# Performance work log

Hardware: AMD Instinct MI355X
Metric: run time of the kernel (lower is better)

The kernel has to match this reference:

```python
import jax, jax.numpy as jnp
from jax import lax
import numpy as np

LATENT = 512
LABEL = 128
BATCH = 1024


def _maxpool2(x):
    # 2x2 max pool, stride 2, NCHW
    return lax.reduce_window(x, -jnp.inf, lax.max, (1, 1, 2, 2), (1, 1, 2, 2), 'VALID')


def _encoder(x, c1w, c1b, c2w, c2b, fw, fb):
    dn = ('NCHW', 'OIHW', 'NCHW')
    y = lax.conv_general_dilated(x, c1w, (1, 1), 'SAME', dimension_numbers=dn)
    y = _maxpool2(jax.nn.relu(y + c1b[None, :, None, None]))  # [B,32,14,14]
    y = lax.conv_general_dilated(y, c2w, (1, 1), 'SAME', dimension_numbers=dn)
    y = _maxpool2(jax.nn.relu(y + c2b[None, :, None, None]))  # [B,64,7,7]
    y = y.reshape(y.shape[0], -1)                              # [B,3136]
    return y @ fw.T + fb                                       # [B,latent]


def _hopfield_w(rep):
    # rho = mean over ALL elements (matches torch.mean(x))
    rho = jnp.mean(rep)
    t = rep - rho                      # [label, latent]
    w = t.T @ t                        # sum of rank-1 outer products
    w = w * (1.0 - jnp.eye(w.shape[0], dtype=w.dtype))  # zero diagonal
    return w / LABEL


def _clustering(lat, w):
    # batched fixed-length Hopfield relaxation with min-energy tracking
    s0 = jnp.tanh(lat)                 # [B,L]
    B = s0.shape[0]

    def step(carry, _):
        s, min_e, min_s = carry
        prev = lax.stop_gradient(s)    # torch detaches prev_s each iter
        s_new = jnp.abs(prev) * jnp.sign(prev @ w.T)      # [B,L]
        e = -jnp.einsum('bi,ij,bj->b', s_new, w, s_new)    # [B]
        better = e < min_e
        min_e = jnp.where(better, e, min_e)
        min_s = jnp.where(better[:, None], s_new, min_s)
        return (s_new, min_e, min_s), None

    init = (s0, jnp.full((B,), jnp.inf, dtype=s0.dtype), jnp.zeros_like(s0))
    (_, _, min_s), _ = lax.scan(step, init, None, length=LATENT)
    return min_s


def setup_inputs() -> dict:
    key = jax.random.key(0)
    ks = jax.random.split(key, 11)
    d = {}
    d['image'] = jax.random.normal(ks[0], (BATCH, 1, 28, 28), dtype=jnp.float32)
    d['label_images'] = jax.random.uniform(ks[1], (LABEL, 1, 28, 28), dtype=jnp.float32)
    d['conv1_w'] = jax.random.normal(ks[2], (32, 1, 5, 5), dtype=jnp.float32) * 0.1
    d['conv1_b'] = jnp.zeros((32,), dtype=jnp.float32)
    d['conv2_w'] = jax.random.normal(ks[3], (64, 32, 5, 5), dtype=jnp.float32) * 0.05
    d['conv2_b'] = jnp.zeros((64,), dtype=jnp.float32)
    d['fc1_w'] = jax.random.normal(ks[4], (LATENT, 64 * 7 * 7), dtype=jnp.float32) * 0.02
    d['fc1_b'] = jnp.zeros((LATENT,), dtype=jnp.float32)
    d['fcn_w'] = jax.random.normal(ks[5], (LABEL, LATENT), dtype=jnp.float32) * 0.05
    d['fcn_b'] = jnp.zeros((LABEL,), dtype=jnp.float32)
    return d


def reference(image, label_images, conv1_w, conv1_b, conv2_w, conv2_b,
              fc1_w, fc1_b, fcn_w, fcn_b):
    rep = jnp.tanh(_encoder(label_images, conv1_w, conv1_b, conv2_w, conv2_b, fc1_w, fc1_b))  # [label,L]
    lat = _encoder(image, conv1_w, conv1_b, conv2_w, conv2_b, fc1_w, fc1_b)                    # [B,L]
    # FCN on detached latents (torch: .clone().detach())
    label = jax.nn.softmax(lax.stop_gradient(lat) @ fcn_w.T + fcn_b, axis=1)                   # [B,label]
    w = _hopfield_w(rep)                                                                        # [L,L]
    min_s = _clustering(lat, w)                                                                 # [B,L]
    out = jax.nn.softmax(jnp.abs(min_s @ rep.T), axis=1)                                        # [B,label]
    return (out, label)
```

## Files before the change

### kernel.cpp

```cpp
#include <hip/hip_runtime.h>
#include <hip/hip_bf16.h>
#include <math.h>

#define BATCH 1024
#define LABEL 128
#define LATENT 512
#define NTOT 1152

typedef short short8 __attribute__((ext_vector_type(8)));
typedef float f32x16 __attribute__((ext_vector_type(16)));

__device__ __forceinline__ unsigned short f2bf(float f) {
    __hip_bfloat16 h = __float2bfloat16(f);
    return *(unsigned short*)&h;
}
__device__ __forceinline__ float bf2f(unsigned short u) {
    __hip_bfloat16 h; *(unsigned short*)&h = u;
    return __bfloat162float(h);
}


__global__ __launch_bounds__(256) void conv1_pool(const float* __restrict__ image,
                                                  const float* __restrict__ limg,
                                                  const float* __restrict__ wt,
                                                  const float* __restrict__ bias,
                                                  unsigned short* __restrict__ o1b) {
    const int n = blockIdx.x;
    const float* in = (n < BATCH) ? (image + (size_t)n * 784)
                                  : (limg + (size_t)(n - BATCH) * 784);
    __shared__ float pin[32][32];
    __shared__ float wts[32 * 25];
    const int tid = threadIdx.x;
    unsigned short* ob = o1b + (size_t)n * 12800;
    for (int i = tid; i < 256; i += 256) {
        int pl_ = i >> 7, r = i & 127;
        ob[pl_ * 6400 + 6272 + r] = 0;
    }
    for (int idx = tid; idx < 32 * 32; idx += 256) ((float*)pin)[idx] = 0.f;
    __syncthreads();
    for (int idx = tid; idx < 784; idx += 256) {
        int y = idx / 28, x = idx % 28;
        pin[y + 2][x + 2] = in[idx];
    }
    for (int idx = tid; idx < 800; idx += 256) wts[idx] = wt[idx];
    __syncthreads();
    const int oc = tid & 31;
    float wk[25];
    #pragma unroll
    for (int k = 0; k < 25; ++k) wk[k] = wts[oc * 25 + k];
    float b = bias[oc];
    const int slot_lo = (oc & 7);
    const int gq = oc >> 3;
    for (int o = tid; o < 6272; o += 256) {
        int p = o >> 5, py = p / 14, px = p % 14;
        float win[6][6];
        #pragma unroll
        for (int r = 0; r < 6; ++r)
        #pragma unroll
        for (int c = 0; c < 6; ++c)
            win[r][c] = pin[2 * py + r][2 * px + c];
        float a00 = b, a01 = b, a10 = b, a11 = b;
        #pragma unroll
        for (int ky = 0; ky < 5; ++ky)
        #pragma unroll
        for (int kx = 0; kx < 5; ++kx) {
            float w = wk[ky * 5 + kx];
            a00 = fmaf(win[ky][kx], w, a00);
            a01 = fmaf(win[ky][kx + 1], w, a01);
            a10 = fmaf(win[ky + 1][kx], w, a10);
            a11 = fmaf(win[ky + 1][kx + 1], w, a11);
        }
        float v = fmaxf(fmaxf(fmaxf(a00, a01), fmaxf(a10, a11)), 0.f);
        unsigned short b1 = f2bf(v); float r1 = v - bf2f(b1);
        unsigned short b2 = f2bf(r1);
        int off = p * 32 + (((gq ^ (p >> 1)) & 3) << 3) + slot_lo;
        ob[off] = b1; ob[6400 + off] = b2;
    }
}

#define BSTR ((size_t)512 * 3136)
#define ASTR ((size_t)NTOT * 3136)
__global__ __launch_bounds__(256) void prep(const float* __restrict__ c2w,
                                            const float* __restrict__ f1w,
                                            unsigned short* __restrict__ Bf,
                                            unsigned short* __restrict__ Bw2) {
    int idx = blockIdx.x * 256 + threadIdx.x;
    if (idx < 102400) {
        int j = idx & 7, lane = (idx >> 3) & 63, ocT = (idx >> 9) & 1, s = idx >> 10;
        int q = lane >> 5, nn = lane & 31;
        int k = 16 * s + 8 * q + j;
        int tap = k >> 5, ic = k & 31;
        int oc = 32 * ocT + nn;
        float v = c2w[oc * 800 + ic * 25 + tap];
        unsigned short b1 = f2bf(v);
        unsigned short b2 = f2bf(v - bf2f(b1));
        size_t base = ((size_t)(s * 2 + ocT) * 2) * 512 + lane * 8 + j;
        Bf[base] = b1; Bf[base + 512] = b2;
        return;
    }
    int i2 = idx - 102400;
    if (i2 >= 512 * 3136) return;
    float v = f1w[i2];
    unsigned short b1 = f2bf(v);
    unsigned short b2 = f2bf(v - bf2f(b1));
    Bw2[i2] = b1; Bw2[BSTR + i2] = b2;
}

__global__ __launch_bounds__(256) void conv2_mfma(const unsigned short* __restrict__ o1b,
                                                  const unsigned short* __restrict__ Bf,
                                                  const float* __restrict__ bias,
                                                  unsigned short* __restrict__ out2) {
    const int n = blockIdx.x;
    __shared__ __align__(16) unsigned short pl[12800];
    const int tid = threadIdx.x;
    const int lane = tid & 63, wv = tid >> 6;
    const int ocT = wv & 1, mh = wv >> 1;

    {
        const float4* src = (const float4*)(o1b + (size_t)n * 12800);
        float4* dst = (float4*)pl;
        for (int i = tid; i < 1600; i += 256) dst[i] = src[i];
    }
    __syncthreads();

    const int m_ = lane & 31, q = lane >> 5;
    int ym[4], xm[4], mm[4], tvv[4];
    #pragma unroll
    for (int tt = 0; tt < 4; ++tt) {
        int t = 4 * mh + tt;
        tvv[tt] = (t < 7);
        int m = 32 * t + m_;
        mm[tt] = m;
        ym[tt] = m / 14;
        xm[tt] = m - 14 * ym[tt];
    }
    f32x16 acc[4];
    {
        float bs = bias[32 * ocT + m_];
        #pragma unroll
        for (int tt = 0; tt < 4; ++tt)
        #pragma unroll
        for (int r = 0; r < 16; ++r) acc[tt][r] = bs;
    }

    for (int s = 0; s < 50; ++s) {
        const unsigned short* bp = Bf + ((size_t)(s * 2 + ocT) * 2) * 512 + lane * 8;
        short8 b1 = *(const short8*)(bp);
        short8 b2 = *(const short8*)(bp + 512);
        int kb = 16 * s + 8 * q;
        int tap = kb >> 5, ic0 = kb & 31, g = ic0 >> 3;
        int ky = (tap * 13) >> 6;
        int kx = tap - ky * 5;
        int iyk = ky - 2, ixk = kx - 2;
        int pq2 = iyk * 14 + ixk;
        short8 a1[4], a2[4];
        #pragma unroll
        for (int tt = 0; tt < 4; ++tt) {
            int iy = ym[tt] + iyk, ix = xm[tt] + ixk;
            int valid = tvv[tt] & ((unsigned)iy < 14u) & ((unsigned)ix < 14u);
            int cpt = valid ? (mm[tt] + pq2) : 196;
            int addr = cpt * 32 + (((g ^ (cpt >> 1)) & 3) << 3);
            a1[tt] = *(const short8*)(pl + addr);
            a2[tt] = *(const short8*)(pl + 6400 + addr);
        }
        #pragma unroll
        for (int tt = 0; tt < 4; ++tt)
            acc[tt] = __builtin_amdgcn_mfma_f32_32x32x16_bf16(a1[tt], b1, acc[tt], 0, 0, 0);
        #pragma unroll
        for (int tt = 0; tt < 4; ++tt)
            acc[tt] = __builtin_amdgcn_mfma_f32_32x32x16_bf16(a1[tt], b2, acc[tt], 0, 0, 0);
        #pragma unroll
        for (int tt = 0; tt < 4; ++tt)
            acc[tt] = __builtin_amdgcn_mfma_f32_32x32x16_bf16(a2[tt], b1, acc[tt], 0, 0, 0);
    }
    __syncthreads();

    float* hx = (float*)pl;
    {
        const int oc = 32 * ocT + m_;
        #pragma unroll
        for (int tt = 0; tt < 4; ++tt)
        #pragma unroll
        for (int e = 0; e < 8; ++e) {
            const int reg = 2 * e;
            const int r = (reg & 3) + 8 * (reg >> 2) + 4 * q;
            const int m = 32 * (4 * mh + tt) + r;
            if (m < 196) {
                float xm2 = fmaxf(acc[tt][reg], acc[tt][reg + 1]);
                int y = (m * 2341) >> 15;
                int px = (m - 14 * y) >> 1;
                hx[(y * 7 + px) * 65 + oc] = xm2;
            }
        }
    }
    __syncthreads();

    for (int idx = tid; idx < 3136; idx += 256) {
        int oc2 = (idx * 2675) >> 17;
        int p = idx - 49 * oc2;
        int py = (p * 9363) >> 16;
        int px = p - 7 * py;
        float v = fmaxf(hx[(2 * py * 7 + px) * 65 + oc2],
                        hx[((2 * py + 1) * 7 + px) * 65 + oc2]);
        v = fmaxf(v, 0.f);
        unsigned short b1 = f2bf(v);
        unsigned short b2 = f2bf(v - bf2f(b1));
        size_t o = (size_t)n * 3136 + idx;
        out2[o] = b1; out2[ASTR + o] = b2;
    }
}

__global__ __launch_bounds__(256) void fc1_mfma(const unsigned short* __restrict__ A2,
                                                const unsigned short* __restrict__ B2,
                                                float* __restrict__ part) {
    __shared__ unsigned short As[2][2048];
    __shared__ unsigned short Bs[2][2048];
    const int tid = threadIdx.x;
    const int n0 = blockIdx.x * 64, m0 = blockIdx.y * 64;
    const int koff = blockIdx.z * 448;
    const int lr = tid >> 2, g = tid & 3;
    const int slot = (((g ^ (lr >> 1)) & 3) << 3);
    const int lane = tid & 63, wv = tid >> 6;
    const int nq = wv & 1, mq = wv >> 1;
    const int q = lane >> 5, l31 = lane & 31;
    const int rA = 32 * nq + l31, rB = 32 * mq + l31;
    f32x16 acc;
    #pragma unroll
    for (int r = 0; r < 16; ++r) acc[r] = 0.f;

    for (int bk = 0; bk < 448; bk += 32) {
        const size_t ka = (size_t)(koff + bk + (g << 3));
        short8 av[2], bv[2];
        #pragma unroll
        for (int p = 0; p < 2; ++p) {
            av[p] = *(const short8*)(A2 + p * ASTR + (size_t)(n0 + lr) * 3136 + ka);
            bv[p] = *(const short8*)(B2 + p * BSTR + (size_t)(m0 + lr) * 3136 + ka);
        }
        __syncthreads();
        #pragma unroll
        for (int p = 0; p < 2; ++p) {
            *(short8*)&As[p][(lr << 5) + slot] = av[p];
            *(short8*)&Bs[p][(lr << 5) + slot] = bv[p];
        }
        __syncthreads();
        #pragma unroll
        for (int s2 = 0; s2 < 32; s2 += 16) {
            const int gg = (s2 + (q << 3)) >> 3;
            const int sa = (((gg ^ (rA >> 1)) & 3) << 3);
            const int sb = (((gg ^ (rB >> 1)) & 3) << 3);
            short8 a1 = *(const short8*)&As[0][(rA << 5) + sa];
            short8 a2 = *(const short8*)&As[1][(rA << 5) + sa];
            short8 b1 = *(const short8*)&Bs[0][(rB << 5) + sb];
            short8 b2 = *(const short8*)&Bs[1][(rB << 5) + sb];
            acc = __builtin_amdgcn_mfma_f32_32x32x16_bf16(a1, b1, acc, 0, 0, 0);
            acc = __builtin_amdgcn_mfma_f32_32x32x16_bf16(a1, b2, acc, 0, 0, 0);
            acc = __builtin_amdgcn_mfma_f32_32x32x16_bf16(a2, b1, acc, 0, 0, 0);
        }
    }
    float* pb = part + (size_t)blockIdx.z * NTOT * 512;
    #pragma unroll
    for (int reg = 0; reg < 16; ++reg) {
        int nn = n0 + 32 * nq + (reg & 3) + 8 * (reg >> 2) + 4 * q;
        int mmo = m0 + 32 * mq + l31;
        pb[(size_t)nn * 512 + mmo] = acc[reg];
    }
}

__global__ __launch_bounds__(256) void fc1_reduce(const float* __restrict__ part,
                                                  const float* __restrict__ bias,
                                                  float* __restrict__ lat,
                                                  float* __restrict__ rep) {
    int idx = blockIdx.x * 256 + threadIdx.x;
    int m = idx & 511;
    float v = bias[m];
    #pragma unroll
    for (int kz = 0; kz < 7; ++kz) v += part[(size_t)kz * NTOT * 512 + idx];
    if (idx < BATCH * 512) lat[idx] = v;
    else rep[idx - BATCH * 512] = tanhf(v);
}

__global__ __launch_bounds__(128) void fcn_softmax(const float* __restrict__ lat,
                                                   const float* __restrict__ fw,
                                                   const float* __restrict__ fb,
                                                   float* __restrict__ out) {
    const int b = blockIdx.x;
    const int j = threadIdx.x;
    __shared__ float lrow[512];
    __shared__ float red[128];
    for (int i = j; i < 512; i += 128) lrow[i] = lat[b * 512 + i];
    __syncthreads();
    const float4* w4 = (const float4*)(fw + j * 512);
    float acc = fb[j];
    #pragma unroll 4
    for (int qq = 0; qq < 128; ++qq) {
        float4 a = ((const float4*)lrow)[qq];
        float4 w = w4[qq];
        acc += a.x * w.x + a.y * w.y + a.z * w.z + a.w * w.w;
    }
    red[j] = acc;
    __syncthreads();
    for (int off = 64; off >= 1; off >>= 1) {
        if (j < off) red[j] = fmaxf(red[j], red[j + off]);
        __syncthreads();
    }
    float mx = red[0];
    __syncthreads();
    float ex = expf(acc - mx);
    red[j] = ex;
    __syncthreads();
    for (int off = 64; off >= 1; off >>= 1) {
        if (j < off) red[j] += red[j + off];
        __syncthreads();
    }
    out[b * 128 + j] = ex / red[0];
}

__global__ __launch_bounds__(256) void rho_kernel(const float* __restrict__ rep,
                                                  float* __restrict__ rho) {
    __shared__ float red[256];
    const int tid = threadIdx.x;
    float s = 0.f;
    for (int i = tid; i < LABEL * LATENT; i += 256) s += rep[i];
    red[tid] = s;
    __syncthreads();
    for (int off = 128; off >= 1; off >>= 1) {
        if (tid < off) red[tid] += red[tid + off];
        __syncthreads();
    }
    if (tid == 0) rho[0] = red[0] / (float)(LABEL * LATENT);
}

__global__ __launch_bounds__(256) void t_kernel(const float* __restrict__ rep,
                                                const float* __restrict__ rho,
                                                float* __restrict__ tT) {
    int idx = blockIdx.x * 256 + threadIdx.x;
    int i = idx / 128, k = idx % 128;
    tT[idx] = rep[k * 512 + i] - rho[0];
}

__global__ __launch_bounds__(256) void w_kernel(const float* __restrict__ tT,
                                                float* __restrict__ w) {
    int idx = blockIdx.x * 256 + threadIdx.x;
    int i = idx >> 9, j = idx & 511;
    const float4* a = (const float4*)(tT + i * 128);
    const float4* b = (const float4*)(tT + j * 128);
    float acc = 0.f;
    #pragma unroll 8
    for (int q = 0; q < 32; ++q) {
        float4 av = a[q], bv = b[q];
        acc += av.x * bv.x + av.y * bv.y + av.z * bv.z + av.w * bv.w;
    }
    w[idx] = (i == j) ? 0.f : acc * (1.f / 128.f);
}

__global__ __launch_bounds__(256) void hinit(const float* __restrict__ lat,
                                             const float* __restrict__ w,
                                             float* __restrict__ hmat) {
    __shared__ float As[16][68];
    __shared__ float Bs[16][68];
    const int tid = threadIdx.x;
    const int n0 = blockIdx.x * 64, m0 = blockIdx.y * 64;
    const int lr = tid >> 2;
    const int lk = (tid & 3) * 4;
    const int ty = tid >> 4, tx = tid & 15;
    float c[4][4] = {};
    for (int k0 = 0; k0 < 512; k0 += 16) {
        float4 a4 = *(const float4*)(lat + (size_t)(n0 + lr) * 512 + k0 + lk);
        float4 b4 = *(const float4*)(w + (size_t)(m0 + lr) * 512 + k0 + lk);
        a4.x = tanhf(a4.x); a4.y = tanhf(a4.y); a4.z = tanhf(a4.z); a4.w = tanhf(a4.w);
        __syncthreads();
        As[lk + 0][lr] = a4.x; As[lk + 1][lr] = a4.y; As[lk + 2][lr] = a4.z; As[lk + 3][lr] = a4.w;
        Bs[lk + 0][lr] = b4.x; Bs[lk + 1][lr] = b4.y; Bs[lk + 2][lr] = b4.z; Bs[lk + 3][lr] = b4.w;
        __syncthreads();
        #pragma unroll
        for (int kk = 0; kk < 16; ++kk) {
            float av[4], bv[4];
            #pragma unroll
            for (int i = 0; i < 4; ++i) av[i] = As[kk][ty * 4 + i];
            #pragma unroll
            for (int j = 0; j < 4; ++j) bv[j] = Bs[kk][tx * 4 + j];
            #pragma unroll
            for (int i = 0; i < 4; ++i)
            #pragma unroll
            for (int j = 0; j < 4; ++j) c[i][j] += av[i] * bv[j];
        }
    }
    #pragma unroll
    for (int i = 0; i < 4; ++i)
    #pragma unroll
    for (int j = 0; j < 4; ++j)
        hmat[(size_t)(n0 + ty * 4 + i) * 512 + m0 + tx * 4 + j] = c[i][j];
}

#define CB 2
__device__ __forceinline__ float sgnf(float x) {
    return (x > 0.f) ? 1.f : ((x < 0.f) ? -1.f : 0.f);
}

__global__ __launch_bounds__(256) void clustering(const float* __restrict__ lat,
                                                  const float* __restrict__ hmat,
                                                  const float* __restrict__ w,
                                                  const float* __restrict__ rep,
                                                  float* __restrict__ out) {
    const int tid = threadIdx.x;
    const int row0 = blockIdx.x * CB;
    __shared__ float mins[CB][512];
    __shared__ float red[256];
    __shared__ float part_e[4][CB];
    __shared__ int part_c[4];
    __shared__ float min_e[CB];
    __shared__ int copyf[CB];
    __shared__ int donef[CB];
    __shared__ int cnt[CB];
    __shared__ int jidx[CB][512];
    __shared__ float jdel[CB][512];
    const int i0 = 2 * tid, i1 = 2 * tid + 1;
    const int wave = tid >> 6, lane = tid & 63;

    float sm10[CB], sm11[CB], sm20[CB], sm21[CB], h0[CB], h1[CB];
    #pragma unroll
    for (int r = 0; r < CB; ++r) {
        float a = tanhf(lat[(row0 + r) * 512 + i0]);
        float b = tanhf(lat[(row0 + r) * 512 + i1]);
        sm10[r] = a; sm11[r] = b;
        sm20[r] = a; sm21[r] = b;
        h0[r] = hmat[(size_t)(row0 + r) * 512 + i0];
        h1[r] = hmat[(size_t)(row0 + r) * 512 + i1];
    }
    if (tid < CB) { min_e[tid] = INFINITY; donef[tid] = 0; cnt[tid] = 0; }
    __syncthreads();

    for (int k = 1; k <= 512; ++k) {
        float sn0[CB], sn1[CB];
        int cy = (1 << CB) - 1;
        #pragma unroll
        for (int r = 0; r < CB; ++r) {
            int dn = donef[r];
            if (dn) {
                sn0[r] = sm10[r]; sn1[r] = sm11[r];
            } else {
                sn0[r] = fabsf(sm10[r]) * sgnf(h0[r]);
                sn1[r] = fabsf(sm11[r]) * sgnf(h1[r]);
                if (!(sn0[r] == sm20[r] && sn1[r] == sm21[r])) cy &= ~(1 << r);
                if (sn0[r] != sm10[r]) {
                    int p = atomicAdd(&cnt[r], 1);
                    jidx[r][p] = i0; jdel[r][p] = sn0[r] - sm10[r];
                }
                if (sn1[r] != sm11[r]) {
                    int p = atomicAdd(&cnt[r], 1);
                    jidx[r][p] = i1; jdel[r][p] = sn1[r] - sm11[r];
                }
            }
        }
        #pragma unroll
        for (int m = 32; m >= 1; m >>= 1) cy &= __shfl_xor(cy, m, 64);
        if (lane == 0) part_c[wave] = cy;
        __syncthreads();

        #pragma unroll
        for (int r = 0; r < CB; ++r) {
            const int c = cnt[r];
            #pragma unroll 4
            for (int t = 0; t < c; ++t) {
                const int j = jidx[r][t];
                const float d = jdel[r][t];
                const float2 wvv = *(const float2*)(w + (size_t)j * 512 + i0);
                h0[r] = fmaf(d, wvv.x, h0[r]);
                h1[r] = fmaf(d, wvv.y, h1[r]);
            }
        }
        float ep[CB];
        #pragma unroll
        for (int r = 0; r < CB; ++r) ep[r] = sn0[r] * h0[r] + sn1[r] * h1[r];
        #pragma unroll
        for (int m = 32; m >= 1; m >>= 1) {
            #pragma unroll
            for (int r = 0; r < CB; ++r) ep[r] += __shfl_xor(ep[r], m, 64);
        }
        if (lane == 0) {
            #pragma unroll
            for (int r = 0; r < CB; ++r) part_e[wave][r] = ep[r];
        }
        __syncthreads();

        if (tid < CB) {
            int r = tid;
            if (!donef[r]) {
                float e = -(part_e[0][r] + part_e[1][r] + part_e[2][r] + part_e[3][r]);
                int better = e < min_e[r];
                if (better) min_e[r] = e;
                copyf[r] = better;
                int fl = part_c[0] & part_c[1] & part_c[2] & part_c[3];
                int fixedp = (cnt[r] == 0);
                int cyc = (k >= 2) && ((fl >> r) & 1);
                if (fixedp || cyc) donef[r] = 1;
            } else {
                copyf[r] = 0;
            }
            cnt[r] = 0;
        }
        __syncthreads();

        int alldone = 1;
        #pragma unroll
        for (int r = 0; r < CB; ++r) {
            if (copyf[r]) { mins[r][i0] = sn0[r]; mins[r][i1] = sn1[r]; }
            alldone &= donef[r];
            sm20[r] = sm10[r]; sm21[r] = sm11[r];
            sm10[r] = sn0[r];  sm11[r] = sn1[r];
        }
        if (alldone) break;
    }
    __syncthreads();

    const int j = tid & 127, half = tid >> 7;
    for (int r = 0; r < CB; ++r) {
        const float4* rr = (const float4*)(rep + (size_t)j * 512 + half * 256);
        const float4* ms = (const float4*)(&mins[r][half * 256]);
        float p = 0.f;
        #pragma unroll 8
        for (int q = 0; q < 64; ++q) {
            float4 rv = rr[q], mv = ms[q];
            p += rv.x * mv.x + rv.y * mv.y + rv.z * mv.z + rv.w * mv.w;
        }
        red[tid] = p;
        __syncthreads();
        float v = 0.f;
        if (tid < 128) { v = fabsf(red[tid] + red[tid + 128]); red[tid] = v; }
        __syncthreads();
        for (int off = 64; off >= 1; off >>= 1) {
            if (tid < off) red[tid] = fmaxf(red[tid], red[tid + off]);
            __syncthreads();
        }
        float mx = red[0];
        __syncthreads();
        float ex = 0.f;
        if (tid < 128) { ex = expf(v - mx); red[tid] = ex; }
        __syncthreads();
        for (int off = 64; off >= 1; off >>= 1) {
            if (tid < off) red[tid] += red[tid + off];
            __syncthreads();
        }
        if (tid < 128) out[(size_t)(row0 + r) * 128 + tid] = ex / red[0];
        __syncthreads();
    }
}

extern "C" void kernel_launch(void* const* d_in, const int* in_sizes, int n_in,
                              void* d_out, int out_size, void* d_ws, size_t ws_size,
                              hipStream_t stream) {
    const float* image = (const float*)d_in[0];
    const float* limg  = (const float*)d_in[1];
    const float* c1w   = (const float*)d_in[2];
    const float* c1b   = (const float*)d_in[3];
    const float* c2w   = (const float*)d_in[4];
    const float* c2b   = (const float*)d_in[5];
    const float* f1w   = (const float*)d_in[6];
    const float* f1b   = (const float*)d_in[7];
    const float* fnw   = (const float*)d_in[8];
    const float* fnb   = (const float*)d_in[9];
    float* out = (float*)d_out;
    float* ws  = (float*)d_ws;

    unsigned short* o1b  = (unsigned short*)ws;
    unsigned short* out2 = o1b + (size_t)NTOT * 12800;
    float* lat  = (float*)(out2 + 2 * ASTR);
    float* rep  = lat + (size_t)BATCH * 512;
    float* tT   = rep + (size_t)LABEL * 512;
    float* wmat = tT + (size_t)512 * 128;
    float* rho  = wmat + (size_t)512 * 512;
    unsigned short* Bw2   = (unsigned short*)(rho + 16);
    unsigned short* Bfrag = Bw2 + 2 * BSTR;
    float* hmat = (float*)(Bfrag + 102400);
    float* part = (float*)ws;

    hipLaunchKernelGGL(prep, dim3((102400 + 512 * 3136 + 255) / 256), dim3(256), 0, stream,
                       c2w, f1w, Bfrag, Bw2);
    hipLaunchKernelGGL(conv1_pool, dim3(NTOT), dim3(256), 0, stream, image, limg, c1w, c1b, o1b);
    hipLaunchKernelGGL(conv2_mfma, dim3(NTOT), dim3(256), 0, stream, o1b, Bfrag, c2b, out2);
    hipLaunchKernelGGL(fc1_mfma, dim3(NTOT / 64, 512 / 64, 7), dim3(256), 0, stream,
                       out2, Bw2, part);
    hipLaunchKernelGGL(fc1_reduce, dim3(NTOT * 512 / 256), dim3(256), 0, stream,
                       part, f1b, lat, rep);
    hipLaunchKernelGGL(fcn_softmax, dim3(BATCH), dim3(128), 0, stream, lat, fnw, fnb,
                       out + (size_t)BATCH * LABEL);
    hipLaunchKernelGGL(rho_kernel, dim3(1), dim3(256), 0, stream, rep, rho);
    hipLaunchKernelGGL(t_kernel, dim3(256), dim3(256), 0, stream, rep, rho, tT);
    hipLaunchKernelGGL(w_kernel, dim3(1024), dim3(256), 0, stream, tT, wmat);
    hipLaunchKernelGGL(hinit, dim3(BATCH / 64, 512 / 64), dim3(256), 0, stream, lat, wmat, hmat);
    hipLaunchKernelGGL(clustering, dim3(BATCH / CB), dim3(256), 0, stream,
                       lat, hmat, wmat, rep, out);
}
```

Before: 422.8 us.

## Row-strip conv1 register blocking and split-bf16 MFMA for FCN logits

```diff
diff --git a/kernel.cpp b/kernel.cpp
--- a/kernel.cpp
+++ b/kernel.cpp
@@ -18,6 +18,11 @@
     __hip_bfloat16 h; *(unsigned short*)&h = u;
     return __bfloat162float(h);
 }
+
+#define BSTR ((size_t)512 * 3136)
+#define ASTR ((size_t)NTOT * 3136)
+#define A2STR ((size_t)BATCH * 512)
+#define W2STR ((size_t)LABEL * 512)
 
 
 __global__ __launch_bounds__(256) void conv1_pool(const float* __restrict__ image,
@@ -48,42 +53,69 @@
     float wk[25];
     #pragma unroll
     for (int k = 0; k < 25; ++k) wk[k] = wts[oc * 25 + k];
-    float b = bias[oc];
+    const float b = bias[oc];
     const int slot_lo = (oc & 7);
     const int gq = oc >> 3;
-    for (int o = tid; o < 6272; o += 256) {
-        int p = o >> 5, py = p / 14, px = p % 14;
-        float win[6][6];
-        #pragma unroll
-        for (int r = 0; r < 6; ++r)
-        #pragma unroll
-        for (int c = 0; c < 6; ++c)
-            win[r][c] = pin[2 * py + r][2 * px + c];
-        float a00 = b, a01 = b, a10 = b, a11 = b;
-        #pragma unroll
-        for (int ky = 0; ky < 5; ++ky)
-        #pragma unroll
-        for (int kx = 0; kx < 5; ++kx) {
-            float w = wk[ky * 5 + kx];
-            a00 = fmaf(win[ky][kx], w, a00);
-            a01 = fmaf(win[ky][kx + 1], w, a01);
-            a10 = fmaf(win[ky + 1][kx], w, a10);
-            a11 = fmaf(win[ky + 1][kx + 1], w, a11);
-        }
-        float v = fmaxf(fmaxf(fmaxf(a00, a01), fmaxf(a10, a11)), 0.f);
-        unsigned short b1 = f2bf(v); float r1 = v - bf2f(b1);
-        unsigned short b2 = f2bf(r1);
-        int off = p * 32 + (((gq ^ (p >> 1)) & 3) << 3) + slot_lo;
-        ob[off] = b1; ob[6400 + off] = b2;
-    }
-}
-
-#define BSTR ((size_t)512 * 3136)
-#define ASTR ((size_t)NTOT * 3136)
+    for (int it = 0; it < 2; ++it) {
+        const int py = (tid >> 5) + it * 8;
+        if (py >= 14) continue;
+        #pragma unroll
+        for (int xh = 0; xh < 2; ++xh) {
+            const int acol = xh ? 12 : 0;
+            const int off = xh ? 2 : 0;
+            float a0[14], a1[14];
+            #pragma unroll
+            for (int c = 0; c < 14; ++c) { a0[c] = b; a1[c] = b; }
+            #pragma unroll
+            for (int t = 0; t < 6; ++t) {
+                float row[20];
+                const float4* rp = (const float4*)&pin[2 * py + t][acol];
+                #pragma unroll
+                for (int v = 0; v < 5; ++v) {
+                    float4 f = rp[v];
+                    row[4 * v] = f.x; row[4 * v + 1] = f.y;
+                    row[4 * v + 2] = f.z; row[4 * v + 3] = f.w;
+                }
+                if (t < 5) {
+                    #pragma unroll
+                    for (int kx = 0; kx < 5; ++kx) {
+                        float w0 = wk[t * 5 + kx];
+                        #pragma unroll
+                        for (int c = 0; c < 14; ++c)
+                            a0[c] = fmaf(row[c + kx + off], w0, a0[c]);
+                    }
+                }
+                if (t >= 1) {
+                    #pragma unroll
+                    for (int kx = 0; kx < 5; ++kx) {
+                        float w1 = wk[(t - 1) * 5 + kx];
+                        #pragma unroll
+                        for (int c = 0; c < 14; ++c)
+                            a1[c] = fmaf(row[c + kx + off], w1, a1[c]);
+                    }
+                }
+            }
+            #pragma unroll
+            for (int px = 0; px < 7; ++px) {
+                float v = fmaxf(fmaxf(a0[2 * px], a0[2 * px + 1]),
+                                fmaxf(a1[2 * px], a1[2 * px + 1]));
+                v = fmaxf(v, 0.f);
+                unsigned short b1 = f2bf(v);
+                unsigned short b2 = f2bf(v - bf2f(b1));
+                int p = py * 14 + 7 * xh + px;
+                int offo = p * 32 + (((gq ^ (p >> 1)) & 3) << 3) + slot_lo;
+                ob[offo] = b1; ob[6400 + offo] = b2;
+            }
+        }
+    }
+}
+
 __global__ __launch_bounds__(256) void prep(const float* __restrict__ c2w,
                                             const float* __restrict__ f1w,
+                                            const float* __restrict__ fnw,
                                             unsigned short* __restrict__ Bf,
-                                            unsigned short* __restrict__ Bw2) {
+                                            unsigned short* __restrict__ Bw2,
+                                            unsigned short* __restrict__ Bn2) {
     int idx = blockIdx.x * 256 + threadIdx.x;
     if (idx < 102400) {
         int j = idx & 7, lane = (idx >> 3) & 63, ocT = (idx >> 9) & 1, s = idx >> 10;
@@ -99,11 +131,19 @@
         return;
     }
     int i2 = idx - 102400;
-    if (i2 >= 512 * 3136) return;
-    float v = f1w[i2];
+    if (i2 < 512 * 3136) {
+        float v = f1w[i2];
+        unsigned short b1 = f2bf(v);
+        unsigned short b2 = f2bf(v - bf2f(b1));
+        Bw2[i2] = b1; Bw2[BSTR + i2] = b2;
+        return;
+    }
+    int i3 = i2 - 512 * 3136;
+    if (i3 >= 128 * 512) return;
+    float v = fnw[i3];
     unsigned short b1 = f2bf(v);
     unsigned short b2 = f2bf(v - bf2f(b1));
-    Bw2[i2] = b1; Bw2[BSTR + i2] = b2;
+    Bn2[i3] = b1; Bn2[W2STR + i3] = b2;
 }
 
 __global__ __launch_bounds__(256) void conv2_mfma(const unsigned short* __restrict__ o1b,
@@ -269,34 +309,84 @@
 __global__ __launch_bounds__(256) void fc1_reduce(const float* __restrict__ part,
                                                   const float* __restrict__ bias,
                                                   float* __restrict__ lat,
+                                                  unsigned short* __restrict__ lat2,
                                                   float* __restrict__ rep) {
     int idx = blockIdx.x * 256 + threadIdx.x;
     int m = idx & 511;
     float v = bias[m];
     #pragma unroll
     for (int kz = 0; kz < 7; ++kz) v += part[(size_t)kz * NTOT * 512 + idx];
-    if (idx < BATCH * 512) lat[idx] = v;
-    else rep[idx - BATCH * 512] = tanhf(v);
-}
-
-__global__ __launch_bounds__(128) void fcn_softmax(const float* __restrict__ lat,
-                                                   const float* __restrict__ fw,
-                                                   const float* __restrict__ fb,
-                                                   float* __restrict__ out) {
+    if (idx < BATCH * 512) {
+        lat[idx] = v;
+        unsigned short b1 = f2bf(v);
+        lat2[idx] = b1;
+        lat2[A2STR + idx] = f2bf(v - bf2f(b1));
+    } else {
+        rep[idx - BATCH * 512] = tanhf(v);
+    }
+}
+
+__global__ __launch_bounds__(256) void fcn_mfma(const unsigned short* __restrict__ A2,
+                                                const unsigned short* __restrict__ B2,
+                                                float* __restrict__ logits) {
+    __shared__ unsigned short As[2][2048];
+    __shared__ unsigned short Bs[2][2048];
+    const int tid = threadIdx.x;
+    const int n0 = blockIdx.x * 64, m0 = blockIdx.y * 64;
+    const int lr = tid >> 2, g = tid & 3;
+    const int slot = (((g ^ (lr >> 1)) & 3) << 3);
+    const int lane = tid & 63, wv = tid >> 6;
+    const int nq = wv & 1, mq = wv >> 1;
+    const int q = lane >> 5, l31 = lane & 31;
+    const int rA = 32 * nq + l31, rB = 32 * mq + l31;
+    f32x16 acc;
+    #pragma unroll
+    for (int r = 0; r < 16; ++r) acc[r] = 0.f;
+
+    for (int bk = 0; bk < 512; bk += 32) {
+        const size_t ka = (size_t)(bk + (g << 3));
+        short8 av[2], bv[2];
+        #pragma unroll
+        for (int p = 0; p < 2; ++p) {
+            av[p] = *(const short8*)(A2 + p * A2STR + (size_t)(n0 + lr) * 512 + ka);
+            bv[p] = *(const short8*)(B2 + p * W2STR + (size_t)(m0 + lr) * 512 + ka);
+        }
+        __syncthreads();
+        #pragma unroll
+        for (int p = 0; p < 2; ++p) {
+            *(short8*)&As[p][(lr << 5) + slot] = av[p];
+            *(short8*)&Bs[p][(lr << 5) + slot] = bv[p];
+        }
+        __syncthreads();
+        #pragma unroll
+        for (int s2 = 0; s2 < 32; s2 += 16) {
+            const int gg = (s2 + (q << 3)) >> 3;
+            const int sa = (((gg ^ (rA >> 1)) & 3) << 3);
+            const int sb = (((gg ^ (rB >> 1)) & 3) << 3);
+            short8 a1 = *(const short8*)&As[0][(rA << 5) + sa];
+            short8 a2 = *(const short8*)&As[1][(rA << 5) + sa];
+            short8 b1 = *(const short8*)&Bs[0][(rB << 5) + sb];
+            short8 b2 = *(const short8*)&Bs[1][(rB << 5) + sb];
+            acc = __builtin_amdgcn_mfma_f32_32x32x16_bf16(a1, b1, acc, 0, 0, 0);
+            acc = __builtin_amdgcn_mfma_f32_32x32x16_bf16(a1, b2, acc, 0, 0, 0);
+            acc = __builtin_amdgcn_mfma_f32_32x32x16_bf16(a2, b1, acc, 0, 0, 0);
+        }
+    }
+    #pragma unroll
+    for (int reg = 0; reg < 16; ++reg) {
+        int nn = n0 + 32 * nq + (reg & 3) + 8 * (reg >> 2) + 4 * q;
+        int mmo = m0 + 32 * mq + l31;
+        logits[(size_t)nn * 128 + mmo] = acc[reg];
+    }
+}
+
+__global__ __launch_bounds__(128) void fcn_softmax2(const float* __restrict__ logits,
+                                                    const float* __restrict__ fb,
+                                                    float* __restrict__ out) {
     const int b = blockIdx.x;
     const int j = threadIdx.x;
-    __shared__ float lrow[512];
     __shared__ float red[128];
-    for (int i = j; i < 512; i += 128) lrow[i] = lat[b * 512 + i];
-    __syncthreads();
-    const float4* w4 = (const float4*)(fw + j * 512);
-    float acc = fb[j];
-    #pragma unroll 4
-    for (int qq = 0; qq < 128; ++qq) {
-        float4 a = ((const float4*)lrow)[qq];
-        float4 w = w4[qq];
-        acc += a.x * w.x + a.y * w.y + a.z * w.z + a.w * w.w;
-    }
+    float acc = logits[(size_t)b * 128 + j] + fb[j];
     red[j] = acc;
     __syncthreads();
     for (int off = 64; off >= 1; off >>= 1) {
@@ -312,7 +402,7 @@
         if (j < off) red[j] += red[j + off];
         __syncthreads();
     }
-    out[b * 128 + j] = ex / red[0];
+    out[(size_t)b * 128 + j] = ex / red[0];
 }
 
 __global__ __launch_bounds__(256) void rho_kernel(const float* __restrict__ rep,
@@ -572,17 +662,22 @@
     unsigned short* Bw2   = (unsigned short*)(rho + 16);
     unsigned short* Bfrag = Bw2 + 2 * BSTR;
     float* hmat = (float*)(Bfrag + 102400);
+    unsigned short* lat2 = (unsigned short*)(hmat + A2STR);
+    unsigned short* fnw2 = lat2 + 2 * A2STR;
+    float* logits = (float*)(fnw2 + 2 * W2STR);
     float* part = (float*)ws;
 
-    hipLaunchKernelGGL(prep, dim3((102400 + 512 * 3136 + 255) / 256), dim3(256), 0, stream,
-                       c2w, f1w, Bfrag, Bw2);
+    const int prep_total = 102400 + 512 * 3136 + 128 * 512;
+    hipLaunchKernelGGL(prep, dim3((prep_total + 255) / 256), dim3(256), 0, stream,
+                       c2w, f1w, fnw, Bfrag, Bw2, fnw2);
     hipLaunchKernelGGL(conv1_pool, dim3(NTOT), dim3(256), 0, stream, image, limg, c1w, c1b, o1b);
     hipLaunchKernelGGL(conv2_mfma, dim3(NTOT), dim3(256), 0, stream, o1b, Bfrag, c2b, out2);
     hipLaunchKernelGGL(fc1_mfma, dim3(NTOT / 64, 512 / 64, 7), dim3(256), 0, stream,
                        out2, Bw2, part);
     hipLaunchKernelGGL(fc1_reduce, dim3(NTOT * 512 / 256), dim3(256), 0, stream,
-                       part, f1b, lat, rep);
-    hipLaunchKernelGGL(fcn_softmax, dim3(BATCH), dim3(128), 0, stream, lat, fnw, fnb,
+                       part, f1b, lat, lat2, rep);
+    hipLaunchKernelGGL(fcn_mfma, dim3(16, 2), dim3(256), 0, stream, lat2, fnw2, logits);
+    hipLaunchKernelGGL(fcn_softmax2, dim3(BATCH), dim3(128), 0, stream, logits, fnb,
                        out + (size_t)BATCH * LABEL);
     hipLaunchKernelGGL(rho_kernel, dim3(1), dim3(256), 0, stream, rep, rho);
     hipLaunchKernelGGL(t_kernel, dim3(256), dim3(256), 0, stream, rep, rho, tT);
```

Measured after the change: 401.2 us. 1.05x faster.
